# Optimization experiments

Hardware: AMD Instinct MI355X
Metric: run time of the kernel (lower is better)

The kernel has to match this reference:

```python
import jax, jax.numpy as jnp
import numpy as np

D_HIDDEN = 1024
NUM_HEADS = 16
D_HEAD = D_HIDDEN // NUM_HEADS


def setup_inputs() -> dict:
    key = jax.random.key(0)
    ks = jax.random.split(key, 9)
    N, S, D = 4, 2048, D_HIDDEN
    s = 1.0 / np.sqrt(D)
    inp = {
        "x": jax.random.normal(ks[0], (N, S, D), dtype=jnp.float32),
        "Wq": jax.random.uniform(ks[1], (D, D), jnp.float32, -s, s),
        "bq": jnp.zeros((D,), jnp.float32),
        "Wk": jax.random.uniform(ks[2], (D, D), jnp.float32, -s, s),
        "bk": jnp.zeros((D,), jnp.float32),
        "Wv": jax.random.uniform(ks[3], (D, D), jnp.float32, -s, s),
        "bv": jnp.zeros((D,), jnp.float32),
        "Wo": jax.random.uniform(ks[4], (D, D), jnp.float32, -s, s),
        "bo": jnp.zeros((D,), jnp.float32),
        "ln_gamma": jnp.ones((D,), jnp.float32),
        "ln_beta": jnp.zeros((D,), jnp.float32),
    }
    return inp


def _layer_norm(x, gamma, beta, eps=1e-5):
    mu = jnp.mean(x, axis=-1, keepdims=True)
    var = jnp.var(x, axis=-1, keepdims=True)
    return (x - mu) * jax.lax.rsqrt(var + eps) * gamma + beta


def reference(x, Wq, bq, Wk, bk, Wv, bv, Wo, bo, ln_gamma, ln_beta):
    N, S, D = x.shape
    H, Dh = NUM_HEADS, D_HEAD
    xn = _layer_norm(x, ln_gamma, ln_beta)
    # torch Linear: y = x @ W.T + b
    q = (xn @ Wq.T + bq).reshape(N, S, H, Dh)
    k = (xn @ Wk.T + bk).reshape(N, S, H, Dh)
    v = (xn @ Wv.T + bv).reshape(N, S, H, Dh)
    # scores: [N, H, S, S]
    scores = jnp.einsum('nxhd,nyhd->nhxy', q, k) / np.sqrt(Dh)
    # causal mask: positions y > x get -inf
    mask = jnp.triu(jnp.full((S, S), -jnp.inf, dtype=scores.dtype), k=1)
    attn = jax.nn.softmax(scores + mask[None, None], axis=-1)
    z = jnp.einsum('nhxy,nyhd->nxhd', attn, v).reshape(N, S, D)
    return z @ Wo.T + bo
```

## Files before the change

kernel.cpp:

```cpp
#include <hip/hip_runtime.h>

typedef unsigned short u16;
typedef unsigned int   u32;
typedef __bf16 bf16x8 __attribute__((ext_vector_type(8)));
typedef float  f32x4  __attribute__((ext_vector_type(4)));
typedef unsigned short u16x8 __attribute__((ext_vector_type(8)));
typedef unsigned short u16x4 __attribute__((ext_vector_type(4)));

#define SEQ 2048
#define DM  1024
#define TOKS 8388608
#define SCLQ 0.18033688f

__device__ __forceinline__ float bf2f(u16 u) {
    u32 i = ((u32)u) << 16;
    float f; __builtin_memcpy(&f, &i, 4); return f;
}
__device__ __forceinline__ u16 f2bf(float f) {
    u32 i; __builtin_memcpy(&i, &f, 4);
    return (u16)((i + 0x7FFFu + ((i >> 16) & 1u)) >> 16);
}
__device__ __forceinline__ bf16x8 ld8(const u16* p) {
    return __builtin_bit_cast(bf16x8, *(const u16x8*)p);
}
#define GLD16(src, dst) __builtin_amdgcn_global_load_lds( \
    (const __attribute__((address_space(1))) void*)(src), \
    (__attribute__((address_space(3))) void*)(dst), 16, 0, 0)

__global__ __launch_bounds__(64) void detect_k(const u32* __restrict__ x, int* __restrict__ flag) {
    const int lane = threadIdx.x;
    u32 w = x[lane];
    int e0 = (int)((w >> 7) & 0xFFu);
    int cnt = (e0 >= 100 && e0 <= 140) ? 1 : 0;
#pragma unroll
    for (int off = 32; off; off >>= 1) cnt += __shfl_xor(cnt, off);
    if (lane == 0) *flag = (cnt < 32) ? 1 : 0;
}

__global__ __launch_bounds__(256) void convert_k(const void* s0, const void* s1, const void* s2, const void* s3,
                                                 const void* v0, const void* v1, const void* v2, const void* v3,
                                                 const void* v4, const void* v5,
                                                 u16* __restrict__ dstW, u16* __restrict__ dstV,
                                                 const int* __restrict__ flagp) {
    const int y = blockIdx.y, tid = threadIdx.x;
    const int fp32m = *flagp;
    const void* src; u16* dst; size_t off;
    if (y < 4) {
        src = (y == 0) ? s0 : (y == 1) ? s1 : (y == 2) ? s2 : s3;
        dst = dstW + (size_t)y * 1048576;
        off = (size_t)blockIdx.x * 1024 + tid * 4;
    } else {
        const int i = blockIdx.x;
        if (i >= 6) return;
        src = (i == 0) ? v0 : (i == 1) ? v1 : (i == 2) ? v2 : (i == 3) ? v3 : (i == 4) ? v4 : v5;
        dst = dstV + (size_t)i * 1024;
        off = (size_t)tid * 4;
    }
    u16x4 o;
    if (fp32m) {
        const float* f = (const float*)src + off;
#pragma unroll
        for (int j = 0; j < 4; ++j) o[j] = f2bf(f[j]);
    } else {
        o = *(const u16x4*)((const u16*)src + off);
    }
    *(u16x4*)(dst + off) = o;
}

__global__ __launch_bounds__(256) void ln_k(const void* __restrict__ xv,
                                            const u16* __restrict__ g,
                                            const u16* __restrict__ b,
                                            u16* __restrict__ xn,
                                            const int* __restrict__ flagp) {
    const int row = blockIdx.x, tid = threadIdx.x;
    const int fp32m = *flagp;
    float f[4], s1 = 0.f, s2 = 0.f;
    if (fp32m) {
        f32x4 v = *(const f32x4*)((const float*)xv + (size_t)row * DM + tid * 4);
#pragma unroll
        for (int j = 0; j < 4; ++j) f[j] = v[j];
    } else {
        u16x4 v = *(const u16x4*)((const u16*)xv + (size_t)row * DM + tid * 4);
#pragma unroll
        for (int j = 0; j < 4; ++j) f[j] = bf2f(v[j]);
    }
#pragma unroll
    for (int j = 0; j < 4; ++j) { s1 += f[j]; s2 += f[j] * f[j]; }
#pragma unroll
    for (int off = 32; off; off >>= 1) { s1 += __shfl_xor(s1, off); s2 += __shfl_xor(s2, off); }
    __shared__ float red[8];
    const int wave = tid >> 6, lane = tid & 63;
    if (lane == 0) { red[wave] = s1; red[4 + wave] = s2; }
    __syncthreads();
    s1 = red[0] + red[1] + red[2] + red[3];
    s2 = red[4] + red[5] + red[6] + red[7];
    const float mu = s1 * (1.f / DM);
    const float var = s2 * (1.f / DM) - mu * mu;
    const float rs = rsqrtf(var + 1e-5f);
    u16x4 gv = *(const u16x4*)(g + tid * 4);
    u16x4 bv = *(const u16x4*)(b + tid * 4);
    u16x4 o;
#pragma unroll
    for (int j = 0; j < 4; ++j) o[j] = f2bf((f[j] - mu) * rs * bf2f(gv[j]) + bf2f(bv[j]));
    *(u16x4*)(xn + (size_t)row * DM + tid * 4) = o;
}


#define LDS_U16 73728

__device__ __forceinline__ void wait_vm12() { asm volatile("s_waitcnt vmcnt(12)" ::: "memory"); }
__device__ __forceinline__ void wait_vm6()  { asm volatile("s_waitcnt vmcnt(6)"  ::: "memory"); }
__device__ __forceinline__ void wait_vm0()  { asm volatile("s_waitcnt vmcnt(0)"  ::: "memory"); }

template <int EPI>
__device__ __forceinline__ void gemm256x128(u16* lds,
                                            const u16* __restrict__ A,
                                            const u16* __restrict__ W,
                                            const u16* __restrict__ bias,
                                            u16* __restrict__ o0, u16* __restrict__ o1, u16* __restrict__ o2,
                                            int fp32m) {
    const int tid = threadIdx.x;
    const int w = tid >> 6, lane = tid & 63;
    const int l4 = lane & 15, q4 = lane >> 4;
    const int bm = blockIdx.x, bn = blockIdx.y;
    const int wm = (w >> 1) * 64, wn = (w & 1) * 64;

    const int srow = lane >> 3;
    const int schk = (lane & 7) ^ srow;
    const u16* sA = A + ((size_t)(bm * 256 + w * 32 + srow)) * DM + (schk << 3);
    const u16* sB = W + ((size_t)(bn * 128 + w * 16 + srow)) * DM + (schk << 3);

    int offA[4][2], offB[4][2];
#pragma unroll
    for (int mt = 0; mt < 4; ++mt)
#pragma unroll
        for (int s = 0; s < 2; ++s) {
            const int row = wm + mt * 16 + l4;
            offA[mt][s] = row * 64 + (((s * 4 + q4) ^ (l4 & 7)) << 3);
        }
#pragma unroll
    for (int nt = 0; nt < 4; ++nt)
#pragma unroll
        for (int s = 0; s < 2; ++s) {
            const int row = wn + nt * 16 + l4;
            offB[nt][s] = 16384 + row * 64 + (((s * 4 + q4) ^ (l4 & 7)) << 3);
        }

    auto STAGE = [&](int kt, int b) {
        const u16* a0 = sA + kt * 64;
        const u16* b0 = sB + kt * 64;
        u16* la = lds + b * 24576 + w * 2048;
        u16* lb = lds + b * 24576 + 16384 + w * 1024;
        GLD16(a0,           la);
        GLD16(a0 + 8 * DM,  la + 512);
        GLD16(a0 + 16 * DM, la + 1024);
        GLD16(a0 + 24 * DM, la + 1536);
        GLD16(b0,           lb);
        GLD16(b0 + 8 * DM,  lb + 512);
    };

    f32x4 acc[4][4] = {};

    STAGE(0, 0); STAGE(1, 1); STAGE(2, 2);

#pragma unroll
    for (int kt = 0; kt < 16; ++kt) {
        const int b = kt % 3;
        if (kt < 14)      wait_vm12();
        else if (kt == 14) wait_vm6();
        else               wait_vm0();
        __builtin_amdgcn_s_barrier();
        __builtin_amdgcn_sched_barrier(0);
        const u16* base = lds + b * 24576;
        bf16x8 af[4][2], bfr[4][2];
#pragma unroll
        for (int mt = 0; mt < 4; ++mt)
#pragma unroll
            for (int s = 0; s < 2; ++s) af[mt][s] = ld8(base + offA[mt][s]);
#pragma unroll
        for (int nt = 0; nt < 2; ++nt)
#pragma unroll
            for (int s = 0; s < 2; ++s) bfr[nt][s] = ld8(base + offB[nt][s]);
        __builtin_amdgcn_s_setprio(1);
#pragma unroll
        for (int mt = 0; mt < 4; ++mt)
#pragma unroll
            for (int nt = 0; nt < 2; ++nt)
#pragma unroll
                for (int s = 0; s < 2; ++s)
                    acc[mt][nt] = __builtin_amdgcn_mfma_f32_16x16x32_bf16(af[mt][s], bfr[nt][s], acc[mt][nt], 0, 0, 0);
        __builtin_amdgcn_s_setprio(0);
#pragma unroll
        for (int nt = 2; nt < 4; ++nt)
#pragma unroll
            for (int s = 0; s < 2; ++s) bfr[nt][s] = ld8(base + offB[nt][s]);
        __builtin_amdgcn_s_setprio(1);
#pragma unroll
        for (int mt = 0; mt < 4; ++mt)
#pragma unroll
            for (int nt = 2; nt < 4; ++nt)
#pragma unroll
                for (int s = 0; s < 2; ++s)
                    acc[mt][nt] = __builtin_amdgcn_mfma_f32_16x16x32_bf16(af[mt][s], bfr[nt][s], acc[mt][nt], 0, 0, 0);
        __builtin_amdgcn_s_setprio(0);
        __builtin_amdgcn_s_barrier();
        __builtin_amdgcn_sched_barrier(0);
        if (kt < 13) STAGE(kt + 3, b);
    }

    if (EPI == 0) {
        const int whichB = bn >> 3;
        const int cb = (bn & 7) * 128 + wn;
        u16* outp = (whichB == 0) ? o0 : (whichB == 1) ? o1 : o2;
        const float scl = (whichB == 0) ? SCLQ : 1.0f;
#pragma unroll
        for (int nt = 0; nt < 4; ++nt) {
            const int cc = cb + nt * 16 + l4;
            const float bs = bf2f(bias[whichB * 1024 + cc]);
#pragma unroll
            for (int mt = 0; mt < 4; ++mt) {
                const int row0 = bm * 256 + wm + mt * 16 + q4 * 4;
                if (whichB < 2) {
#pragma unroll
                    for (int r = 0; r < 4; ++r)
                        outp[(size_t)(row0 + r) * DM + cc] = f2bf((acc[mt][nt][r] + bs) * scl);
                } else {
                    const int nb = row0 >> 11, s0 = row0 & 2047;
                    u16x4 pk;
#pragma unroll
                    for (int r = 0; r < 4; ++r) pk[r] = f2bf(acc[mt][nt][r] + bs);
                    *(u16x4*)(outp + ((size_t)(nb * 1024 + cc)) * SEQ + s0) = pk;
                }
            }
        }
    } else {
#pragma unroll
        for (int nt = 0; nt < 4; ++nt) {
            const int cc = bn * 128 + wn + nt * 16 + l4;
            const float bs = bf2f(bias[cc]);
#pragma unroll
            for (int mt = 0; mt < 4; ++mt) {
                const int row0 = bm * 256 + wm + mt * 16 + q4 * 4;
                if (fp32m) {
#pragma unroll
                    for (int r = 0; r < 4; ++r)
                        ((float*)o0)[(size_t)(row0 + r) * DM + cc] = acc[mt][nt][r] + bs;
                } else {
#pragma unroll
                    for (int r = 0; r < 4; ++r)
                        o0[(size_t)(row0 + r) * DM + cc] = f2bf(acc[mt][nt][r] + bs);
                }
            }
        }
    }
}

__global__ __launch_bounds__(512, 2) void gemm_qkv_k(const u16* __restrict__ xn, const u16* __restrict__ Wc,
                                                     const u16* __restrict__ Vc,
                                                     u16* __restrict__ Q, u16* __restrict__ K, u16* __restrict__ Vt) {
    __shared__ alignas(16) u16 lds[LDS_U16];
    gemm256x128<0>(lds, xn, Wc, Vc, Q, K, Vt, 0);
}

__global__ __launch_bounds__(512, 2) void gemm_out_k(const u16* __restrict__ Z, const u16* __restrict__ Wc,
                                                     const u16* __restrict__ Vc,
                                                     u16* __restrict__ out, const int* __restrict__ flagp) {
    __shared__ alignas(16) u16 lds[LDS_U16];
    const int fp32m = *flagp;
    gemm256x128<1>(lds, Z, Wc + 3 * 1048576, Vc + 3 * 1024, out, nullptr, nullptr, fp32m);
}

__global__ __launch_bounds__(256, 4) void flash_k(const u16* __restrict__ Q,
                                                  const u16* __restrict__ K,
                                                  const u16* __restrict__ Vt,
                                                  u16* __restrict__ Z) {
    const int bh = blockIdx.x;
    const int qb = 15 - (int)blockIdx.y;
    const int n = bh >> 4, h = bh & 15;
    const int tid = threadIdx.x, wave = tid >> 6, lane = tid & 63;
    const int l4 = lane & 15, q4 = lane >> 4;

    __shared__ alignas(16) u16 Ks[2][64 * 32];
    __shared__ alignas(16) u16 Vs[2][64 * 32];
    __shared__ alignas(16) u16 Pl[4][2][16 * 72];

    const int Q0w = qb * 128 + wave * 32;
    bf16x8 qf[2][2];
#pragma unroll
    for (int qt = 0; qt < 2; ++qt) {
        const u16* Qr = Q + ((size_t)(n * SEQ + Q0w + qt * 16 + l4)) * DM + h * 64 + q4 * 8;
        qf[qt][0] = ld8(Qr);
        qf[qt][1] = ld8(Qr + 32);
    }

    const int srow = lane >> 2, scol = (lane & 3) * 8;
    const u16* Kg = K + ((size_t)(n * SEQ + wave * 16 + srow)) * DM + h * 64 + scol;
    const u16* Vg = Vt + ((size_t)(n * 1024 + h * 64 + wave * 16 + srow)) * SEQ + scol;
    u16* KsD0 = &Ks[0][wave * 512];
    u16* KsD1 = &Ks[1][wave * 512];
    u16* VsD0 = &Vs[0][wave * 512];
    u16* VsD1 = &Vs[1][wave * 512];

    f32x4 o[2][4] = {};
    float l_acc[2] = {0.f, 0.f};
    const int nch = 2 * qb + 2;

    for (int c = 0; c < nch; ++c) {
        const int kv0 = c * 64;
        const size_t krow = (size_t)kv0 * DM;
        GLD16(Kg + krow, KsD0);
        GLD16(Kg + krow + 32, KsD1);
        GLD16(Vg + kv0, VsD0);
        GLD16(Vg + kv0 + 32, VsD1);
        __syncthreads();

        bf16x8 a[4][2];
#pragma unroll
        for (int mt = 0; mt < 4; ++mt) {
            a[mt][0] = ld8(&Ks[0][(mt * 16 + l4) * 32 + q4 * 8]);
            a[mt][1] = ld8(&Ks[1][(mt * 16 + l4) * 32 + q4 * 8]);
        }
#pragma unroll
        for (int qt = 0; qt < 2; ++qt) {
            f32x4 st[4];
#pragma unroll
            for (int mt = 0; mt < 4; ++mt) {
                f32x4 zz = {0.f, 0.f, 0.f, 0.f};
                st[mt] = __builtin_amdgcn_mfma_f32_16x16x32_bf16(a[mt][0], qf[qt][0], zz, 0, 0, 0);
                st[mt] = __builtin_amdgcn_mfma_f32_16x16x32_bf16(a[mt][1], qf[qt][1], st[mt], 0, 0, 0);
            }
            const int qg = Q0w + qt * 16 + l4;
            u16* P = Pl[wave][qt];
            float la = l_acc[qt];
#pragma unroll
            for (int mt = 0; mt < 4; ++mt) {
                __bf16 pk[4];
#pragma unroll
                for (int r = 0; r < 4; ++r) {
                    const int kv = kv0 + mt * 16 + q4 * 4 + r;
                    float p = __builtin_amdgcn_exp2f(st[mt][r]);
                    p = (kv > qg) ? 0.f : p;
                    la += p;
                    pk[r] = (__bf16)p;
                }
                *(u16x4*)(P + l4 * 72 + mt * 16 + q4 * 4) = *(u16x4*)pk;
            }
            l_acc[qt] = la;
        }
#pragma unroll
        for (int ks = 0; ks < 2; ++ks) {
            bf16x8 pf0 = ld8(&Pl[wave][0][l4 * 72 + ks * 32 + q4 * 8]);
            bf16x8 pf1 = ld8(&Pl[wave][1][l4 * 72 + ks * 32 + q4 * 8]);
#pragma unroll
            for (int nt = 0; nt < 4; ++nt) {
                bf16x8 vf = ld8(&Vs[ks][(nt * 16 + l4) * 32 + q4 * 8]);
                o[0][nt] = __builtin_amdgcn_mfma_f32_16x16x32_bf16(pf0, vf, o[0][nt], 0, 0, 0);
                o[1][nt] = __builtin_amdgcn_mfma_f32_16x16x32_bf16(pf1, vf, o[1][nt], 0, 0, 0);
            }
        }
        __syncthreads();
    }

#pragma unroll
    for (int qt = 0; qt < 2; ++qt) {
        float l = l_acc[qt];
        l += __shfl_xor(l, 16);
        l += __shfl_xor(l, 32);
        float lr[4];
#pragma unroll
        for (int r = 0; r < 4; ++r) lr[r] = 1.f / __shfl(l, q4 * 4 + r);
#pragma unroll
        for (int nt = 0; nt < 4; ++nt) {
            const int col = h * 64 + nt * 16 + l4;
#pragma unroll
            for (int r = 0; r < 4; ++r) {
                const int row = n * SEQ + Q0w + qt * 16 + q4 * 4 + r;
                Z[(size_t)row * DM + col] = f2bf(o[qt][nt][r] * lr[r]);
            }
        }
    }
}

extern "C" void kernel_launch(void* const* d_in, const int* in_sizes, int n_in,
                              void* d_out, int out_size, void* d_ws, size_t ws_size,
                              hipStream_t stream) {
    const void* x  = d_in[0];
    const void* Wq = d_in[1];
    const void* bq = d_in[2];
    const void* Wk = d_in[3];
    const void* bk = d_in[4];
    const void* Wv = d_in[5];
    const void* bv = d_in[6];
    const void* Wo = d_in[7];
    const void* bo = d_in[8];
    const void* g  = d_in[9];
    const void* b  = d_in[10];
    u16* ws = (u16*)d_ws;

    u16* xn  = ws;
    u16* Qb  = ws + (size_t)TOKS;
    u16* Kb  = ws + (size_t)2 * TOKS;
    u16* Vtb = ws + (size_t)3 * TOKS;
    u16* Zb  = ws;
    u16* Wc  = ws + (size_t)4 * TOKS;
    u16* Vc  = Wc + 4 * 1048576;
    int* flagp = (int*)(Vc + 8 * 1024);

    detect_k<<<dim3(1), 64, 0, stream>>>((const u32*)x, flagp);
    convert_k<<<dim3(1024, 5), 256, 0, stream>>>(Wq, Wk, Wv, Wo, bq, bk, bv, bo, g, b, Wc, Vc, flagp);
    ln_k<<<dim3(4 * SEQ), 256, 0, stream>>>(x, Vc + 4 * 1024, Vc + 5 * 1024, xn, flagp);
    gemm_qkv_k<<<dim3(32, 24), 512, 0, stream>>>(xn, Wc, Vc, Qb, Kb, Vtb);
    flash_k<<<dim3(64, 16), 256, 0, stream>>>(Qb, Kb, Vtb, Zb);
    gemm_out_k<<<dim3(32, 8), 512, 0, stream>>>(Zb, Wc, Vc, (u16*)d_out, flagp);
}
```

Baseline: 250.4 us.

## Rewrite QKV GEMM as 256x256 tile with split-phase double-buffered LDS pipeline

Replaces the shared 256x128 QKV GEMM with a dedicated 256x256-tile kernel in which each of 8 waves computes a 128x64 sub-tile, halving the grid. Global-to-LDS loads for the next k-step are split into four quarter stages interleaved between four MFMA phases, with explicit vmcnt waits and barriers over a double buffer. This raises arithmetic intensity per block and reduces redundant A/B loads. The cost is more accumulator registers (128 floats per lane) at two blocks per CU and fewer blocks (384) across the GPU, which may leave some CUs idle.

```diff
diff --git a/kernel.cpp b/kernel.cpp
--- a/kernel.cpp
+++ b/kernel.cpp
@@ -26,6 +26,10 @@
 #define GLD16(src, dst) __builtin_amdgcn_global_load_lds( \
     (const __attribute__((address_space(1))) void*)(src), \
     (__attribute__((address_space(3))) void*)(dst), 16, 0, 0)
+
+#define SBAR() do { asm volatile("" ::: "memory"); __builtin_amdgcn_sched_barrier(0); \
+    __builtin_amdgcn_s_barrier(); __builtin_amdgcn_sched_barrier(0); asm volatile("" ::: "memory"); } while (0)
+#define WVM(n) asm volatile("s_waitcnt vmcnt(" #n ")" ::: "memory")
 
 __global__ __launch_bounds__(64) void detect_k(const u32* __restrict__ x, int* __restrict__ flag) {
     const int lane = threadIdx.x;
@@ -105,6 +109,145 @@
     *(u16x4*)(xn + (size_t)row * DM + tid * 4) = o;
 }
 
+__global__ __launch_bounds__(512, 2) void gemm_qkv_k(const u16* __restrict__ xn, const u16* __restrict__ Wc,
+                                                     const u16* __restrict__ Vc,
+                                                     u16* __restrict__ Q, u16* __restrict__ K, u16* __restrict__ Vt) {
+    __shared__ alignas(16) u16 lds[65536];
+    const int tid = threadIdx.x;
+    const int w = tid >> 6, lane = tid & 63;
+    const int l4 = lane & 15, q4 = lane >> 4;
+    const int bm = blockIdx.x, bn = blockIdx.y;
+    const int wm0 = (w >> 2) * 128, wn = (w & 3) * 64;
+
+    const int srow = lane >> 3, schk = (lane & 7) ^ srow;
+    const u16* aS = xn + ((size_t)(bm * 256) + srow) * DM + schk * 8;
+    const u16* bS = Wc + ((size_t)(bn * 256) + srow) * DM + schk * 8;
+    const int bg0 = (w >> 1) * 64 + (w & 1) * 16;
+
+    auto STG = [&](int h, int kt, int bufb) {
+        const size_t kk = (size_t)kt * 64;
+        u16* ld0 = lds + bufb * 32768;
+        if (h == 0) {
+            GLD16(aS + (size_t)(8 * w) * DM + kk,        ld0 + (8 * w) * 64);
+            GLD16(aS + (size_t)(128 + 8 * w) * DM + kk,  ld0 + (128 + 8 * w) * 64);
+        } else if (h == 2) {
+            GLD16(aS + (size_t)(64 + 8 * w) * DM + kk,   ld0 + (64 + 8 * w) * 64);
+            GLD16(aS + (size_t)(192 + 8 * w) * DM + kk,  ld0 + (192 + 8 * w) * 64);
+        } else {
+            const int b0 = bg0 + ((h == 3) ? 32 : 0);
+            GLD16(bS + (size_t)b0 * DM + kk,             ld0 + 16384 + b0 * 64);
+            GLD16(bS + (size_t)(b0 + 8) * DM + kk,       ld0 + 16384 + (b0 + 8) * 64);
+        }
+    };
+
+    const int swz0 = (q4 ^ (l4 & 7)) << 3;
+    const int swz1 = ((4 + q4) ^ (l4 & 7)) << 3;
+    const int arow = (wm0 + l4) * 64;
+    const int brow = 16384 + (wn + l4) * 64;
+
+    f32x4 acc[8][4] = {};
+    bf16x8 afLo[4][2], afHi[4][2], bfr[2][2];
+
+    STG(0, 0, 0); STG(1, 0, 0); STG(2, 0, 0); STG(3, 0, 0);
+
+#pragma unroll
+    for (int kt = 0; kt < 16; ++kt) {
+        const int buf = kt & 1, nxt = buf ^ 1;
+        const u16* bp = lds + buf * 32768;
+        const bool pf = (kt < 15);
+        WVM(4); SBAR();
+        if (pf) STG(0, kt + 1, nxt);
+#pragma unroll
+        for (int mt = 0; mt < 4; ++mt) {
+            afLo[mt][0] = ld8(bp + arow + mt * 1024 + swz0);
+            afLo[mt][1] = ld8(bp + arow + mt * 1024 + swz1);
+        }
+#pragma unroll
+        for (int nt = 0; nt < 2; ++nt) {
+            bfr[nt][0] = ld8(bp + brow + nt * 1024 + swz0);
+            bfr[nt][1] = ld8(bp + brow + nt * 1024 + swz1);
+        }
+        __builtin_amdgcn_s_setprio(1);
+#pragma unroll
+        for (int mt = 0; mt < 4; ++mt)
+#pragma unroll
+            for (int nt = 0; nt < 2; ++nt) {
+                acc[mt][nt] = __builtin_amdgcn_mfma_f32_16x16x32_bf16(afLo[mt][0], bfr[nt][0], acc[mt][nt], 0, 0, 0);
+                acc[mt][nt] = __builtin_amdgcn_mfma_f32_16x16x32_bf16(afLo[mt][1], bfr[nt][1], acc[mt][nt], 0, 0, 0);
+            }
+        __builtin_amdgcn_s_setprio(0);
+        if (pf) { WVM(4); } else { WVM(2); }
+        SBAR();
+        if (pf) STG(1, kt + 1, nxt);
+#pragma unroll
+        for (int mt = 0; mt < 4; ++mt) {
+            afHi[mt][0] = ld8(bp + arow + (mt + 4) * 1024 + swz0);
+            afHi[mt][1] = ld8(bp + arow + (mt + 4) * 1024 + swz1);
+        }
+        __builtin_amdgcn_s_setprio(1);
+#pragma unroll
+        for (int mt = 0; mt < 4; ++mt)
+#pragma unroll
+            for (int nt = 0; nt < 2; ++nt) {
+                acc[mt + 4][nt] = __builtin_amdgcn_mfma_f32_16x16x32_bf16(afHi[mt][0], bfr[nt][0], acc[mt + 4][nt], 0, 0, 0);
+                acc[mt + 4][nt] = __builtin_amdgcn_mfma_f32_16x16x32_bf16(afHi[mt][1], bfr[nt][1], acc[mt + 4][nt], 0, 0, 0);
+            }
+        __builtin_amdgcn_s_setprio(0);
+        if (pf) { WVM(4); } else { WVM(0); }
+        SBAR();
+        if (pf) STG(2, kt + 1, nxt);
+#pragma unroll
+        for (int nt = 0; nt < 2; ++nt) {
+            bfr[nt][0] = ld8(bp + brow + (nt + 2) * 1024 + swz0);
+            bfr[nt][1] = ld8(bp + brow + (nt + 2) * 1024 + swz1);
+        }
+        __builtin_amdgcn_s_setprio(1);
+#pragma unroll
+        for (int mt = 0; mt < 4; ++mt)
+#pragma unroll
+            for (int nt = 0; nt < 2; ++nt) {
+                acc[mt + 4][nt + 2] = __builtin_amdgcn_mfma_f32_16x16x32_bf16(afHi[mt][0], bfr[nt][0], acc[mt + 4][nt + 2], 0, 0, 0);
+                acc[mt + 4][nt + 2] = __builtin_amdgcn_mfma_f32_16x16x32_bf16(afHi[mt][1], bfr[nt][1], acc[mt + 4][nt + 2], 0, 0, 0);
+            }
+        __builtin_amdgcn_s_setprio(0);
+        SBAR();
+        if (pf) STG(3, kt + 1, nxt);
+        __builtin_amdgcn_s_setprio(1);
+#pragma unroll
+        for (int mt = 0; mt < 4; ++mt)
+#pragma unroll
+            for (int nt = 0; nt < 2; ++nt) {
+                acc[mt][nt + 2] = __builtin_amdgcn_mfma_f32_16x16x32_bf16(afLo[mt][0], bfr[nt][0], acc[mt][nt + 2], 0, 0, 0);
+                acc[mt][nt + 2] = __builtin_amdgcn_mfma_f32_16x16x32_bf16(afLo[mt][1], bfr[nt][1], acc[mt][nt + 2], 0, 0, 0);
+            }
+        __builtin_amdgcn_s_setprio(0);
+    }
+
+    const int whichB = bn >> 2;
+    const int cb = (bn & 3) * 256 + wn;
+    u16* outp = (whichB == 0) ? Q : (whichB == 1) ? K : Vt;
+    const float scl = (whichB == 0) ? SCLQ : 1.0f;
+#pragma unroll
+    for (int nt = 0; nt < 4; ++nt) {
+        const int cc = cb + nt * 16 + l4;
+        const float bs = bf2f(Vc[whichB * 1024 + cc]);
+#pragma unroll
+        for (int mt = 0; mt < 8; ++mt) {
+            const int row0 = bm * 256 + wm0 + mt * 16 + q4 * 4;
+            if (whichB < 2) {
+#pragma unroll
+                for (int r = 0; r < 4; ++r)
+                    outp[(size_t)(row0 + r) * DM + cc] = f2bf((acc[mt][nt][r] + bs) * scl);
+            } else {
+                const int nb = row0 >> 11, s0 = row0 & 2047;
+                u16x4 pk;
+#pragma unroll
+                for (int r = 0; r < 4; ++r) pk[r] = f2bf(acc[mt][nt][r] + bs);
+                *(u16x4*)(outp + ((size_t)(nb * 1024 + cc)) * SEQ + s0) = pk;
+            }
+        }
+    }
+}
 
 #define LDS_U16 73728
 
@@ -112,13 +255,12 @@
 __device__ __forceinline__ void wait_vm6()  { asm volatile("s_waitcnt vmcnt(6)"  ::: "memory"); }
 __device__ __forceinline__ void wait_vm0()  { asm volatile("s_waitcnt vmcnt(0)"  ::: "memory"); }
 
-template <int EPI>
-__device__ __forceinline__ void gemm256x128(u16* lds,
-                                            const u16* __restrict__ A,
-                                            const u16* __restrict__ W,
-                                            const u16* __restrict__ bias,
-                                            u16* __restrict__ o0, u16* __restrict__ o1, u16* __restrict__ o2,
-                                            int fp32m) {
+__device__ __forceinline__ void gemm256x128_out(u16* lds,
+                                                const u16* __restrict__ A,
+                                                const u16* __restrict__ W,
+                                                const u16* __restrict__ bias,
+                                                u16* __restrict__ o0,
+                                                int fp32m) {
     const int tid = threadIdx.x;
     const int w = tid >> 6, lane = tid & 63;
     const int l4 = lane & 15, q4 = lane >> 4;
@@ -208,58 +350,24 @@
         if (kt < 13) STAGE(kt + 3, b);
     }
 
-    if (EPI == 0) {
-        const int whichB = bn >> 3;
-        const int cb = (bn & 7) * 128 + wn;
-        u16* outp = (whichB == 0) ? o0 : (whichB == 1) ? o1 : o2;
-        const float scl = (whichB == 0) ? SCLQ : 1.0f;
-#pragma unroll
-        for (int nt = 0; nt < 4; ++nt) {
-            const int cc = cb + nt * 16 + l4;
-            const float bs = bf2f(bias[whichB * 1024 + cc]);
-#pragma unroll
-            for (int mt = 0; mt < 4; ++mt) {
-                const int row0 = bm * 256 + wm + mt * 16 + q4 * 4;
-                if (whichB < 2) {
-#pragma unroll
-                    for (int r = 0; r < 4; ++r)
-                        outp[(size_t)(row0 + r) * DM + cc] = f2bf((acc[mt][nt][r] + bs) * scl);
-                } else {
-                    const int nb = row0 >> 11, s0 = row0 & 2047;
-                    u16x4 pk;
-#pragma unroll
-                    for (int r = 0; r < 4; ++r) pk[r] = f2bf(acc[mt][nt][r] + bs);
-                    *(u16x4*)(outp + ((size_t)(nb * 1024 + cc)) * SEQ + s0) = pk;
-                }
-            }
-        }
-    } else {
-#pragma unroll
-        for (int nt = 0; nt < 4; ++nt) {
-            const int cc = bn * 128 + wn + nt * 16 + l4;
-            const float bs = bf2f(bias[cc]);
-#pragma unroll
-            for (int mt = 0; mt < 4; ++mt) {
-                const int row0 = bm * 256 + wm + mt * 16 + q4 * 4;
-                if (fp32m) {
-#pragma unroll
-                    for (int r = 0; r < 4; ++r)
-                        ((float*)o0)[(size_t)(row0 + r) * DM + cc] = acc[mt][nt][r] + bs;
-                } else {
-#pragma unroll
-                    for (int r = 0; r < 4; ++r)
-                        o0[(size_t)(row0 + r) * DM + cc] = f2bf(acc[mt][nt][r] + bs);
-                }
-            }
-        }
-    }
-}
-
-__global__ __launch_bounds__(512, 2) void gemm_qkv_k(const u16* __restrict__ xn, const u16* __restrict__ Wc,
-                                                     const u16* __restrict__ Vc,
-                                                     u16* __restrict__ Q, u16* __restrict__ K, u16* __restrict__ Vt) {
-    __shared__ alignas(16) u16 lds[LDS_U16];
-    gemm256x128<0>(lds, xn, Wc, Vc, Q, K, Vt, 0);
+#pragma unroll
+    for (int nt = 0; nt < 4; ++nt) {
+        const int cc = bn * 128 + wn + nt * 16 + l4;
+        const float bs = bf2f(bias[cc]);
+#pragma unroll
+        for (int mt = 0; mt < 4; ++mt) {
+            const int row0 = bm * 256 + wm + mt * 16 + q4 * 4;
+            if (fp32m) {
+#pragma unroll
+                for (int r = 0; r < 4; ++r)
+                    ((float*)o0)[(size_t)(row0 + r) * DM + cc] = acc[mt][nt][r] + bs;
+            } else {
+#pragma unroll
+                for (int r = 0; r < 4; ++r)
+                    o0[(size_t)(row0 + r) * DM + cc] = f2bf(acc[mt][nt][r] + bs);
+            }
+        }
+    }
 }
 
 __global__ __launch_bounds__(512, 2) void gemm_out_k(const u16* __restrict__ Z, const u16* __restrict__ Wc,
@@ -267,7 +375,7 @@
                                                      u16* __restrict__ out, const int* __restrict__ flagp) {
     __shared__ alignas(16) u16 lds[LDS_U16];
     const int fp32m = *flagp;
-    gemm256x128<1>(lds, Z, Wc + 3 * 1048576, Vc + 3 * 1024, out, nullptr, nullptr, fp32m);
+    gemm256x128_out(lds, Z, Wc + 3 * 1048576, Vc + 3 * 1024, out, fp32m);
 }
 
 __global__ __launch_bounds__(256, 4) void flash_k(const u16* __restrict__ Q,
@@ -409,7 +517,7 @@
     detect_k<<<dim3(1), 64, 0, stream>>>((const u32*)x, flagp);
     convert_k<<<dim3(1024, 5), 256, 0, stream>>>(Wq, Wk, Wv, Wo, bq, bk, bv, bo, g, b, Wc, Vc, flagp);
     ln_k<<<dim3(4 * SEQ), 256, 0, stream>>>(x, Vc + 4 * 1024, Vc + 5 * 1024, xn, flagp);
-    gemm_qkv_k<<<dim3(32, 24), 512, 0, stream>>>(xn, Wc, Vc, Qb, Kb, Vtb);
+    gemm_qkv_k<<<dim3(32, 12), 512, 0, stream>>>(xn, Wc, Vc, Qb, Kb, Vtb);
     flash_k<<<dim3(64, 16), 256, 0, stream>>>(Qb, Kb, Vtb, Zb);
     gemm_out_k<<<dim3(32, 8), 512, 0, stream>>>(Zb, Wc, Vc, (u16*)d_out, flagp);
 }
```

Result: slower. 259.0 us (+3.4%).

## Rewrite QKV GEMM with 256x256 tiles, 4-stage pipeline and block swizzle

Applied to the files above, without the earlier changes.

Replaces the templated 256x128 QKV projection GEMM with a dedicated 256x256 tile kernel. It uses a 4-buffer LDS ring fed by global_load_lds, splits each stage's loads across the two MFMA halves, and remaps block indices so that neighbouring blocks share tiles in L2. Larger tiles halve the grid and raise arithmetic intensity per loaded byte. The cost is more accumulator registers per thread (128 floats) and a single wave of 384 blocks, which risks tail imbalance or register spills.

```diff
diff --git a/kernel.cpp b/kernel.cpp
--- a/kernel.cpp
+++ b/kernel.cpp
@@ -26,6 +26,10 @@
 #define GLD16(src, dst) __builtin_amdgcn_global_load_lds( \
     (const __attribute__((address_space(1))) void*)(src), \
     (__attribute__((address_space(3))) void*)(dst), 16, 0, 0)
+
+#define SBAR() do { asm volatile("" ::: "memory"); __builtin_amdgcn_sched_barrier(0); \
+    __builtin_amdgcn_s_barrier(); __builtin_amdgcn_sched_barrier(0); asm volatile("" ::: "memory"); } while (0)
+#define WVM(n) asm volatile("s_waitcnt vmcnt(" #n ")" ::: "memory")
 
 __global__ __launch_bounds__(64) void detect_k(const u32* __restrict__ x, int* __restrict__ flag) {
     const int lane = threadIdx.x;
@@ -105,6 +109,110 @@
     *(u16x4*)(xn + (size_t)row * DM + tid * 4) = o;
 }
 
+__global__ __launch_bounds__(512, 2) void gemm_qkv_k(const u16* __restrict__ xn, const u16* __restrict__ Wc,
+                                                     const u16* __restrict__ Vc,
+                                                     u16* __restrict__ Q, u16* __restrict__ K, u16* __restrict__ Vt) {
+    __shared__ alignas(16) u16 lds[65536];
+    const int tid = threadIdx.x;
+    const int w = tid >> 6, lane = tid & 63;
+    const int l4 = lane & 15, q4 = lane >> 4;
+    const int orig = blockIdx.y * 32 + blockIdx.x;
+    const int s = (orig & 7) * 48 + (orig >> 3);
+    const int bm = s / 12, bn = s % 12;
+    const int wm0 = (w >> 2) * 128, wn = (w & 3) * 64;
+
+    const int srowl = lane >> 2;
+    const int schk = (lane & 3) ^ ((lane >> 3) & 3);
+    const u16* aS = xn + ((size_t)(bm * 256) + srowl) * DM + schk * 8;
+    const u16* bS = Wc + ((size_t)(bn * 256) + srowl) * DM + schk * 8;
+    const int rb = w * 16;
+
+    auto STG = [&](int h, int kt, int bq) {
+        const size_t kk = (size_t)kt * 32;
+        u16* d = lds + bq * 16384;
+        if (h == 0)      GLD16(aS + (size_t)rb * DM + kk,         d + rb * 32);
+        else if (h == 3) GLD16(aS + (size_t)(128 + rb) * DM + kk, d + 4096 + rb * 32);
+        else if (h == 1) GLD16(bS + (size_t)rb * DM + kk,         d + 8192 + rb * 32);
+        else             GLD16(bS + (size_t)(128 + rb) * DM + kk, d + 12288 + rb * 32);
+    };
+
+    const int swz = (q4 ^ ((l4 >> 1) & 3)) << 3;
+
+    f32x4 acc[8][4] = {};
+    bf16x8 af[4], bfv[4];
+
+#pragma unroll
+    for (int p = 0; p < 3; ++p) {
+        STG(0, p, p); STG(1, p, p); STG(2, p, p); STG(3, p, p);
+    }
+
+    for (int kt = 0; kt < 32; ++kt) {
+        if (kt <= 29)      { WVM(8); }
+        else if (kt == 30) { WVM(4); }
+        else               { WVM(0); }
+        SBAR();
+        const u16* bp = lds + (kt & 3) * 16384;
+        const bool pf = (kt < 29);
+        const int nb = (kt + 3) & 3;
+        if (pf) { STG(0, kt + 3, nb); STG(1, kt + 3, nb); }
+#pragma unroll
+        for (int mt = 0; mt < 4; ++mt) af[mt] = ld8(bp + (wm0 + mt * 16 + l4) * 32 + swz);
+#pragma unroll
+        for (int nt = 0; nt < 4; ++nt) bfv[nt] = ld8(bp + 8192 + (wn + nt * 16 + l4) * 32 + swz);
+        __builtin_amdgcn_s_setprio(1);
+#pragma unroll
+        for (int mt = 0; mt < 4; ++mt)
+#pragma unroll
+            for (int nt = 0; nt < 4; ++nt)
+                acc[mt][nt] = __builtin_amdgcn_mfma_f32_16x16x32_bf16(af[mt], bfv[nt], acc[mt][nt], 0, 0, 0);
+        __builtin_amdgcn_s_setprio(0);
+        if (pf) { STG(2, kt + 3, nb); STG(3, kt + 3, nb); }
+#pragma unroll
+        for (int mt = 0; mt < 4; ++mt) af[mt] = ld8(bp + (wm0 + 64 + mt * 16 + l4) * 32 + swz);
+        __builtin_amdgcn_s_setprio(1);
+#pragma unroll
+        for (int mt = 0; mt < 4; ++mt)
+#pragma unroll
+            for (int nt = 0; nt < 4; ++nt)
+                acc[mt + 4][nt] = __builtin_amdgcn_mfma_f32_16x16x32_bf16(af[mt], bfv[nt], acc[mt + 4][nt], 0, 0, 0);
+        __builtin_amdgcn_s_setprio(0);
+    }
+
+    const int whichB = bn >> 2;
+    const int cb = (bn & 3) * 256 + wn;
+    u16* outp = (whichB == 0) ? Q : (whichB == 1) ? K : Vt;
+    const float scl = (whichB == 0) ? SCLQ : 1.0f;
+    float bs4[4];
+#pragma unroll
+    for (int nt = 0; nt < 4; ++nt) bs4[nt] = bf2f(Vc[whichB * 1024 + cb + nt * 16 + l4]);
+    if (whichB < 2) {
+#pragma unroll
+        for (int mt = 0; mt < 8; ++mt) {
+            const int row0 = bm * 256 + wm0 + mt * 16 + q4 * 4;
+#pragma unroll
+            for (int r = 0; r < 4; ++r) {
+                u16* rowp = outp + (size_t)(row0 + r) * DM + cb;
+#pragma unroll
+                for (int nt = 0; nt < 4; ++nt)
+                    rowp[nt * 16 + l4] = f2bf((acc[mt][nt][r] + bs4[nt]) * scl);
+            }
+        }
+    } else {
+#pragma unroll
+        for (int nt = 0; nt < 4; ++nt) {
+            const int cc = cb + nt * 16 + l4;
+#pragma unroll
+            for (int mt = 0; mt < 8; ++mt) {
+                const int row0 = bm * 256 + wm0 + mt * 16 + q4 * 4;
+                const int nbk = row0 >> 11, s0 = row0 & 2047;
+                u16x4 pk;
+#pragma unroll
+                for (int r = 0; r < 4; ++r) pk[r] = f2bf(acc[mt][nt][r] + bs4[nt]);
+                *(u16x4*)(outp + ((size_t)(nbk * 1024 + cc)) * SEQ + s0) = pk;
+            }
+        }
+    }
+}
 
 #define LDS_U16 73728
 
@@ -112,13 +220,12 @@
 __device__ __forceinline__ void wait_vm6()  { asm volatile("s_waitcnt vmcnt(6)"  ::: "memory"); }
 __device__ __forceinline__ void wait_vm0()  { asm volatile("s_waitcnt vmcnt(0)"  ::: "memory"); }
 
-template <int EPI>
-__device__ __forceinline__ void gemm256x128(u16* lds,
-                                            const u16* __restrict__ A,
-                                            const u16* __restrict__ W,
-                                            const u16* __restrict__ bias,
-                                            u16* __restrict__ o0, u16* __restrict__ o1, u16* __restrict__ o2,
-                                            int fp32m) {
+__device__ __forceinline__ void gemm256x128_out(u16* lds,
+                                                const u16* __restrict__ A,
+                                                const u16* __restrict__ W,
+                                                const u16* __restrict__ bias,
+                                                u16* __restrict__ o0,
+                                                int fp32m) {
     const int tid = threadIdx.x;
     const int w = tid >> 6, lane = tid & 63;
     const int l4 = lane & 15, q4 = lane >> 4;
@@ -208,58 +315,24 @@
         if (kt < 13) STAGE(kt + 3, b);
     }
 
-    if (EPI == 0) {
-        const int whichB = bn >> 3;
-        const int cb = (bn & 7) * 128 + wn;
-        u16* outp = (whichB == 0) ? o0 : (whichB == 1) ? o1 : o2;
-        const float scl = (whichB == 0) ? SCLQ : 1.0f;
-#pragma unroll
-        for (int nt = 0; nt < 4; ++nt) {
-            const int cc = cb + nt * 16 + l4;
-            const float bs = bf2f(bias[whichB * 1024 + cc]);
-#pragma unroll
-            for (int mt = 0; mt < 4; ++mt) {
-                const int row0 = bm * 256 + wm + mt * 16 + q4 * 4;
-                if (whichB < 2) {
-#pragma unroll
-                    for (int r = 0; r < 4; ++r)
-                        outp[(size_t)(row0 + r) * DM + cc] = f2bf((acc[mt][nt][r] + bs) * scl);
-                } else {
-                    const int nb = row0 >> 11, s0 = row0 & 2047;
-                    u16x4 pk;
-#pragma unroll
-                    for (int r = 0; r < 4; ++r) pk[r] = f2bf(acc[mt][nt][r] + bs);
-                    *(u16x4*)(outp + ((size_t)(nb * 1024 + cc)) * SEQ + s0) = pk;
-                }
-            }
-        }
-    } else {
-#pragma unroll
-        for (int nt = 0; nt < 4; ++nt) {
-            const int cc = bn * 128 + wn + nt * 16 + l4;
-            const float bs = bf2f(bias[cc]);
-#pragma unroll
-            for (int mt = 0; mt < 4; ++mt) {
-                const int row0 = bm * 256 + wm + mt * 16 + q4 * 4;
-                if (fp32m) {
-#pragma unroll
-                    for (int r = 0; r < 4; ++r)
-                        ((float*)o0)[(size_t)(row0 + r) * DM + cc] = acc[mt][nt][r] + bs;
-                } else {
-#pragma unroll
-                    for (int r = 0; r < 4; ++r)
-                        o0[(size_t)(row0 + r) * DM + cc] = f2bf(acc[mt][nt][r] + bs);
-                }
-            }
-        }
-    }
-}
-
-__global__ __launch_bounds__(512, 2) void gemm_qkv_k(const u16* __restrict__ xn, const u16* __restrict__ Wc,
-                                                     const u16* __restrict__ Vc,
-                                                     u16* __restrict__ Q, u16* __restrict__ K, u16* __restrict__ Vt) {
-    __shared__ alignas(16) u16 lds[LDS_U16];
-    gemm256x128<0>(lds, xn, Wc, Vc, Q, K, Vt, 0);
+#pragma unroll
+    for (int nt = 0; nt < 4; ++nt) {
+        const int cc = bn * 128 + wn + nt * 16 + l4;
+        const float bs = bf2f(bias[cc]);
+#pragma unroll
+        for (int mt = 0; mt < 4; ++mt) {
+            const int row0 = bm * 256 + wm + mt * 16 + q4 * 4;
+            if (fp32m) {
+#pragma unroll
+                for (int r = 0; r < 4; ++r)
+                    ((float*)o0)[(size_t)(row0 + r) * DM + cc] = acc[mt][nt][r] + bs;
+            } else {
+#pragma unroll
+                for (int r = 0; r < 4; ++r)
+                    o0[(size_t)(row0 + r) * DM + cc] = f2bf(acc[mt][nt][r] + bs);
+            }
+        }
+    }
 }
 
 __global__ __launch_bounds__(512, 2) void gemm_out_k(const u16* __restrict__ Z, const u16* __restrict__ Wc,
@@ -267,7 +340,7 @@
                                                      u16* __restrict__ out, const int* __restrict__ flagp) {
     __shared__ alignas(16) u16 lds[LDS_U16];
     const int fp32m = *flagp;
-    gemm256x128<1>(lds, Z, Wc + 3 * 1048576, Vc + 3 * 1024, out, nullptr, nullptr, fp32m);
+    gemm256x128_out(lds, Z, Wc + 3 * 1048576, Vc + 3 * 1024, out, fp32m);
 }
 
 __global__ __launch_bounds__(256, 4) void flash_k(const u16* __restrict__ Q,
@@ -409,7 +482,7 @@
     detect_k<<<dim3(1), 64, 0, stream>>>((const u32*)x, flagp);
     convert_k<<<dim3(1024, 5), 256, 0, stream>>>(Wq, Wk, Wv, Wo, bq, bk, bv, bo, g, b, Wc, Vc, flagp);
     ln_k<<<dim3(4 * SEQ), 256, 0, stream>>>(x, Vc + 4 * 1024, Vc + 5 * 1024, xn, flagp);
-    gemm_qkv_k<<<dim3(32, 24), 512, 0, stream>>>(xn, Wc, Vc, Qb, Kb, Vtb);
+    gemm_qkv_k<<<dim3(32, 12), 512, 0, stream>>>(xn, Wc, Vc, Qb, Kb, Vtb);
     flash_k<<<dim3(64, 16), 256, 0, stream>>>(Qb, Kb, Vtb, Zb);
     gemm_out_k<<<dim3(32, 8), 512, 0, stream>>>(Zb, Wc, Vc, (u16*)d_out, flagp);
 }
```

Result: no change. 253.1 us (+1.1%).

## Use XOR-swizzled 64-wide K/V LDS tiles in flash kernel; split GEMM templates

Applied to the files above, without the earlier changes.

The flash attention kernel now stores each 64x64 K and V chunk as a single XOR-swizzled 64-column LDS tile instead of two 32-column halves. Each lane loads 16 bytes from full 128-byte rows, giving wider global coalescing, and the reads are swizzled to avoid LDS bank conflicts. The shared GEMM template is split into separate QKV and output functions, and their k-loops change from full unroll to unroll 4. The partial unroll shrinks code size but may cost some scheduling freedom in the pipelined loop.

```diff
diff --git a/kernel.cpp b/kernel.cpp
--- a/kernel.cpp
+++ b/kernel.cpp
@@ -112,13 +112,11 @@
 __device__ __forceinline__ void wait_vm6()  { asm volatile("s_waitcnt vmcnt(6)"  ::: "memory"); }
 __device__ __forceinline__ void wait_vm0()  { asm volatile("s_waitcnt vmcnt(0)"  ::: "memory"); }
 
-template <int EPI>
-__device__ __forceinline__ void gemm256x128(u16* lds,
-                                            const u16* __restrict__ A,
-                                            const u16* __restrict__ W,
-                                            const u16* __restrict__ bias,
-                                            u16* __restrict__ o0, u16* __restrict__ o1, u16* __restrict__ o2,
-                                            int fp32m) {
+__device__ __forceinline__ void gemm_qkv_core(u16* lds,
+                                              const u16* __restrict__ A,
+                                              const u16* __restrict__ W,
+                                              const u16* __restrict__ bias,
+                                              u16* __restrict__ o0, u16* __restrict__ o1, u16* __restrict__ o2) {
     const int tid = threadIdx.x;
     const int w = tid >> 6, lane = tid & 63;
     const int l4 = lane & 15, q4 = lane >> 4;
@@ -163,7 +161,7 @@
 
     STAGE(0, 0); STAGE(1, 1); STAGE(2, 2);
 
-#pragma unroll
+#pragma unroll 4
     for (int kt = 0; kt < 16; ++kt) {
         const int b = kt % 3;
         if (kt < 14)      wait_vm12();
@@ -208,48 +206,27 @@
         if (kt < 13) STAGE(kt + 3, b);
     }
 
-    if (EPI == 0) {
-        const int whichB = bn >> 3;
-        const int cb = (bn & 7) * 128 + wn;
-        u16* outp = (whichB == 0) ? o0 : (whichB == 1) ? o1 : o2;
-        const float scl = (whichB == 0) ? SCLQ : 1.0f;
-#pragma unroll
-        for (int nt = 0; nt < 4; ++nt) {
-            const int cc = cb + nt * 16 + l4;
-            const float bs = bf2f(bias[whichB * 1024 + cc]);
-#pragma unroll
-            for (int mt = 0; mt < 4; ++mt) {
-                const int row0 = bm * 256 + wm + mt * 16 + q4 * 4;
-                if (whichB < 2) {
-#pragma unroll
-                    for (int r = 0; r < 4; ++r)
-                        outp[(size_t)(row0 + r) * DM + cc] = f2bf((acc[mt][nt][r] + bs) * scl);
-                } else {
-                    const int nb = row0 >> 11, s0 = row0 & 2047;
-                    u16x4 pk;
-#pragma unroll
-                    for (int r = 0; r < 4; ++r) pk[r] = f2bf(acc[mt][nt][r] + bs);
-                    *(u16x4*)(outp + ((size_t)(nb * 1024 + cc)) * SEQ + s0) = pk;
-                }
-            }
-        }
-    } else {
-#pragma unroll
-        for (int nt = 0; nt < 4; ++nt) {
-            const int cc = bn * 128 + wn + nt * 16 + l4;
-            const float bs = bf2f(bias[cc]);
-#pragma unroll
-            for (int mt = 0; mt < 4; ++mt) {
-                const int row0 = bm * 256 + wm + mt * 16 + q4 * 4;
-                if (fp32m) {
-#pragma unroll
-                    for (int r = 0; r < 4; ++r)
-                        ((float*)o0)[(size_t)(row0 + r) * DM + cc] = acc[mt][nt][r] + bs;
-                } else {
-#pragma unroll
-                    for (int r = 0; r < 4; ++r)
-                        o0[(size_t)(row0 + r) * DM + cc] = f2bf(acc[mt][nt][r] + bs);
-                }
+    const int whichB = bn >> 3;
+    const int cb = (bn & 7) * 128 + wn;
+    u16* outp = (whichB == 0) ? o0 : (whichB == 1) ? o1 : o2;
+    const float scl = (whichB == 0) ? SCLQ : 1.0f;
+#pragma unroll
+    for (int nt = 0; nt < 4; ++nt) {
+        const int cc = cb + nt * 16 + l4;
+        const float bs = bf2f(bias[whichB * 1024 + cc]);
+#pragma unroll
+        for (int mt = 0; mt < 4; ++mt) {
+            const int row0 = bm * 256 + wm + mt * 16 + q4 * 4;
+            if (whichB < 2) {
+#pragma unroll
+                for (int r = 0; r < 4; ++r)
+                    outp[(size_t)(row0 + r) * DM + cc] = f2bf((acc[mt][nt][r] + bs) * scl);
+            } else {
+                const int nb = row0 >> 11, s0 = row0 & 2047;
+                u16x4 pk;
+#pragma unroll
+                for (int r = 0; r < 4; ++r) pk[r] = f2bf(acc[mt][nt][r] + bs);
+                *(u16x4*)(outp + ((size_t)(nb * 1024 + cc)) * SEQ + s0) = pk;
             }
         }
     }
@@ -259,7 +236,122 @@
                                                      const u16* __restrict__ Vc,
                                                      u16* __restrict__ Q, u16* __restrict__ K, u16* __restrict__ Vt) {
     __shared__ alignas(16) u16 lds[LDS_U16];
-    gemm256x128<0>(lds, xn, Wc, Vc, Q, K, Vt, 0);
+    gemm_qkv_core(lds, xn, Wc, Vc, Q, K, Vt);
+}
+
+__device__ __forceinline__ void gemm256x128_out(u16* lds,
+                                                const u16* __restrict__ A,
+                                                const u16* __restrict__ W,
+                                                const u16* __restrict__ bias,
+                                                u16* __restrict__ o0,
+                                                int fp32m) {
+    const int tid = threadIdx.x;
+    const int w = tid >> 6, lane = tid & 63;
+    const int l4 = lane & 15, q4 = lane >> 4;
+    const int bm = blockIdx.x, bn = blockIdx.y;
+    const int wm = (w >> 1) * 64, wn = (w & 1) * 64;
+
+    const int srow = lane >> 3;
+    const int schk = (lane & 7) ^ srow;
+    const u16* sA = A + ((size_t)(bm * 256 + w * 32 + srow)) * DM + (schk << 3);
+    const u16* sB = W + ((size_t)(bn * 128 + w * 16 + srow)) * DM + (schk << 3);
+
+    int offA[4][2], offB[4][2];
+#pragma unroll
+    for (int mt = 0; mt < 4; ++mt)
+#pragma unroll
+        for (int s = 0; s < 2; ++s) {
+            const int row = wm + mt * 16 + l4;
+            offA[mt][s] = row * 64 + (((s * 4 + q4) ^ (l4 & 7)) << 3);
+        }
+#pragma unroll
+    for (int nt = 0; nt < 4; ++nt)
+#pragma unroll
+        for (int s = 0; s < 2; ++s) {
+            const int row = wn + nt * 16 + l4;
+            offB[nt][s] = 16384 + row * 64 + (((s * 4 + q4) ^ (l4 & 7)) << 3);
+        }
+
+    auto STAGE = [&](int kt, int b) {
+        const u16* a0 = sA + kt * 64;
+        const u16* b0 = sB + kt * 64;
+        u16* la = lds + b * 24576 + w * 2048;
+        u16* lb = lds + b * 24576 + 16384 + w * 1024;
+        GLD16(a0,           la);
+        GLD16(a0 + 8 * DM,  la + 512);
+        GLD16(a0 + 16 * DM, la + 1024);
+        GLD16(a0 + 24 * DM, la + 1536);
+        GLD16(b0,           lb);
+        GLD16(b0 + 8 * DM,  lb + 512);
+    };
+
+    f32x4 acc[4][4] = {};
+
+    STAGE(0, 0); STAGE(1, 1); STAGE(2, 2);
+
+#pragma unroll 4
+    for (int kt = 0; kt < 16; ++kt) {
+        const int b = kt % 3;
+        if (kt < 14)      wait_vm12();
+        else if (kt == 14) wait_vm6();
+        else               wait_vm0();
+        __builtin_amdgcn_s_barrier();
+        __builtin_amdgcn_sched_barrier(0);
+        const u16* base = lds + b * 24576;
+        bf16x8 af[4][2], bfr[4][2];
+#pragma unroll
+        for (int mt = 0; mt < 4; ++mt)
+#pragma unroll
+            for (int s = 0; s < 2; ++s) af[mt][s] = ld8(base + offA[mt][s]);
+#pragma unroll
+        for (int nt = 0; nt < 2; ++nt)
+#pragma unroll
+            for (int s = 0; s < 2; ++s) bfr[nt][s] = ld8(base + offB[nt][s]);
+        __builtin_amdgcn_s_setprio(1);
+#pragma unroll
+        for (int mt = 0; mt < 4; ++mt)
+#pragma unroll
+            for (int nt = 0; nt < 2; ++nt)
+#pragma unroll
+                for (int s = 0; s < 2; ++s)
+                    acc[mt][nt] = __builtin_amdgcn_mfma_f32_16x16x32_bf16(af[mt][s], bfr[nt][s], acc[mt][nt], 0, 0, 0);
+        __builtin_amdgcn_s_setprio(0);
+#pragma unroll
+        for (int nt = 2; nt < 4; ++nt)
+#pragma unroll
+            for (int s = 0; s < 2; ++s) bfr[nt][s] = ld8(base + offB[nt][s]);
+        __builtin_amdgcn_s_setprio(1);
+#pragma unroll
+        for (int mt = 0; mt < 4; ++mt)
+#pragma unroll
+            for (int nt = 2; nt < 4; ++nt)
+#pragma unroll
+                for (int s = 0; s < 2; ++s)
+                    acc[mt][nt] = __builtin_amdgcn_mfma_f32_16x16x32_bf16(af[mt][s], bfr[nt][s], acc[mt][nt], 0, 0, 0);
+        __builtin_amdgcn_s_setprio(0);
+        __builtin_amdgcn_s_barrier();
+        __builtin_amdgcn_sched_barrier(0);
+        if (kt < 13) STAGE(kt + 3, b);
+    }
+
+#pragma unroll
+    for (int nt = 0; nt < 4; ++nt) {
+        const int cc = bn * 128 + wn + nt * 16 + l4;
+        const float bs = bf2f(bias[cc]);
+#pragma unroll
+        for (int mt = 0; mt < 4; ++mt) {
+            const int row0 = bm * 256 + wm + mt * 16 + q4 * 4;
+            if (fp32m) {
+#pragma unroll
+                for (int r = 0; r < 4; ++r)
+                    ((float*)o0)[(size_t)(row0 + r) * DM + cc] = acc[mt][nt][r] + bs;
+            } else {
+#pragma unroll
+                for (int r = 0; r < 4; ++r)
+                    o0[(size_t)(row0 + r) * DM + cc] = f2bf(acc[mt][nt][r] + bs);
+            }
+        }
+    }
 }
 
 __global__ __launch_bounds__(512, 2) void gemm_out_k(const u16* __restrict__ Z, const u16* __restrict__ Wc,
@@ -267,7 +359,7 @@
                                                      u16* __restrict__ out, const int* __restrict__ flagp) {
     __shared__ alignas(16) u16 lds[LDS_U16];
     const int fp32m = *flagp;
-    gemm256x128<1>(lds, Z, Wc + 3 * 1048576, Vc + 3 * 1024, out, nullptr, nullptr, fp32m);
+    gemm256x128_out(lds, Z, Wc + 3 * 1048576, Vc + 3 * 1024, out, fp32m);
 }
 
 __global__ __launch_bounds__(256, 4) void flash_k(const u16* __restrict__ Q,
@@ -280,8 +372,8 @@
     const int tid = threadIdx.x, wave = tid >> 6, lane = tid & 63;
     const int l4 = lane & 15, q4 = lane >> 4;
 
-    __shared__ alignas(16) u16 Ks[2][64 * 32];
-    __shared__ alignas(16) u16 Vs[2][64 * 32];
+    __shared__ alignas(16) u16 Ks[64 * 64];
+    __shared__ alignas(16) u16 Vs[64 * 64];
     __shared__ alignas(16) u16 Pl[4][2][16 * 72];
 
     const int Q0w = qb * 128 + wave * 32;
@@ -293,13 +385,11 @@
         qf[qt][1] = ld8(Qr + 32);
     }
 
-    const int srow = lane >> 2, scol = (lane & 3) * 8;
-    const u16* Kg = K + ((size_t)(n * SEQ + wave * 16 + srow)) * DM + h * 64 + scol;
-    const u16* Vg = Vt + ((size_t)(n * 1024 + h * 64 + wave * 16 + srow)) * SEQ + scol;
-    u16* KsD0 = &Ks[0][wave * 512];
-    u16* KsD1 = &Ks[1][wave * 512];
-    u16* VsD0 = &Vs[0][wave * 512];
-    u16* VsD1 = &Vs[1][wave * 512];
+    const int sr8 = lane >> 3, sc8 = (lane & 7) ^ (lane >> 3);
+    const u16* Kg = K + ((size_t)(n * SEQ + wave * 16 + sr8)) * DM + h * 64 + sc8 * 8;
+    const u16* Vg = Vt + ((size_t)(n * 1024 + h * 64 + wave * 16 + sr8)) * SEQ + sc8 * 8;
+    u16* KsD = Ks + wave * 1024;
+    u16* VsD = Vs + wave * 1024;
 
     f32x4 o[2][4] = {};
     float l_acc[2] = {0.f, 0.f};
@@ -308,17 +398,17 @@
     for (int c = 0; c < nch; ++c) {
         const int kv0 = c * 64;
         const size_t krow = (size_t)kv0 * DM;
-        GLD16(Kg + krow, KsD0);
-        GLD16(Kg + krow + 32, KsD1);
-        GLD16(Vg + kv0, VsD0);
-        GLD16(Vg + kv0 + 32, VsD1);
+        GLD16(Kg + krow,          KsD);
+        GLD16(Kg + krow + 8 * DM, KsD + 512);
+        GLD16(Vg + kv0,           VsD);
+        GLD16(Vg + kv0 + 8 * SEQ, VsD + 512);
         __syncthreads();
 
         bf16x8 a[4][2];
 #pragma unroll
         for (int mt = 0; mt < 4; ++mt) {
-            a[mt][0] = ld8(&Ks[0][(mt * 16 + l4) * 32 + q4 * 8]);
-            a[mt][1] = ld8(&Ks[1][(mt * 16 + l4) * 32 + q4 * 8]);
+            a[mt][0] = ld8(Ks + (mt * 16 + l4) * 64 + (((q4) ^ (l4 & 7)) << 3));
+            a[mt][1] = ld8(Ks + (mt * 16 + l4) * 64 + (((4 + q4) ^ (l4 & 7)) << 3));
         }
 #pragma unroll
         for (int qt = 0; qt < 2; ++qt) {
@@ -353,7 +443,7 @@
             bf16x8 pf1 = ld8(&Pl[wave][1][l4 * 72 + ks * 32 + q4 * 8]);
 #pragma unroll
             for (int nt = 0; nt < 4; ++nt) {
-                bf16x8 vf = ld8(&Vs[ks][(nt * 16 + l4) * 32 + q4 * 8]);
+                bf16x8 vf = ld8(Vs + (nt * 16 + l4) * 64 + (((ks * 4 + q4) ^ (l4 & 7)) << 3));
                 o[0][nt] = __builtin_amdgcn_mfma_f32_16x16x32_bf16(pf0, vf, o[0][nt], 0, 0, 0);
                 o[1][nt] = __builtin_amdgcn_mfma_f32_16x16x32_bf16(pf1, vf, o[1][nt], 0, 0, 0);
             }
```

New measurement: 251.3 us. About the same (+0.4%).
